# Optimization experiments

Hardware: AMD Instinct MI355X
Metric: run time of the kernel (lower is better)

Reference implementation:

```python
import jax, jax.numpy as jnp
import numpy as np

H = 128  # target_size / hidden_size
D_IN = 2  # input_size - 2 (stard_LSTM slices off last 2 grid coords)
SAMP = 10  # sampling_num (hardcoded stride 10 in forward loop)


def lstm_encode(x, lengths, W_ih, W_hh, b_ih, b_hh):
    # x: [B, T, D_IN]; torch.nn.LSTMCell math, zero initial state
    B, T, _ = x.shape
    xg = jnp.einsum('btd,gd->btg', x, W_ih) + b_ih  # precompute input projections [B,T,4H]

    def step(carry, xt):
        h, c = carry
        g = xt + h @ W_hh.T + b_hh
        i, f, gg, o = jnp.split(g, 4, axis=-1)
        c = jax.nn.sigmoid(f) * c + jax.nn.sigmoid(i) * jnp.tanh(gg)
        h = jax.nn.sigmoid(o) * jnp.tanh(c)
        return (h, c), h

    h0 = jnp.zeros((B, H), x.dtype)
    _, hs = jax.lax.scan(step, (h0, h0), xg.transpose(1, 0, 2))
    outputs = hs.transpose(1, 0, 2)  # [B, T, H]
    emb = outputs[jnp.arange(B), jnp.clip(lengths - 1, 0)]  # last valid step per sequence
    return emb, outputs


def gather_sub(tensor, sub_len):
    # tensor: [B, T, H]; sub_len: [B*SAMP]; row k reads tensor[k//SAMP, sub_len[k]-1]
    rows = jnp.arange(sub_len.shape[0]) // SAMP
    return tensor[rows, jnp.clip(sub_len - 1, 0)]


def exp_neg_dist(a, b):
    return jnp.exp(-jnp.sqrt(jnp.sum((a - b) ** 2, axis=-1)))


def setup_inputs() -> dict:
    key = jax.random.key(0)
    ks = jax.random.split(key, 12)
    B, T, D = 220, 512, 4
    NS = B * SAMP
    rint = lambda k, n: jnp.maximum(jax.random.randint(k, (n,), 0, T), 1).astype(jnp.int64)
    inp = {
        'traj_input': jax.random.normal(ks[0], (B, T, D), jnp.float32),
        'traj_length': rint(ks[1], B),
        'traj_anchor_sub_length': rint(ks[2], NS),
        'traj_farest_sub_length': rint(ks[3], NS),
        'traj_anchor_input': jax.random.normal(ks[4], (B, T, D), jnp.float32),
        'traj_anchor_length': rint(ks[5], B),
        'anchor_sub_length': rint(ks[6], NS),
        'traj_farest_input': jax.random.normal(ks[7], (B, T, D), jnp.float32),
        'traj_farest_length': rint(ks[8], B),
        'farest_sub_length': rint(ks[9], NS),
        'W_ih': jax.random.normal(ks[10], (4 * H, D_IN), jnp.float32) / np.sqrt(H),
        'W_hh': jax.random.normal(ks[11], (4 * H, H), jnp.float32) / np.sqrt(H),
        'b_ih': jnp.zeros((4 * H,), jnp.float32),
        'b_hh': jnp.zeros((4 * H,), jnp.float32),
    }
    return inp


def reference(traj_input, traj_length, traj_anchor_sub_length, traj_farest_sub_length,
              traj_anchor_input, traj_anchor_length, anchor_sub_length,
              traj_farest_input, traj_farest_length, farest_sub_length,
              W_ih, W_hh, b_ih, b_hh):
    # stard_LSTM=True path: cell input drops last 2 coords
    t_emb, t_out = lstm_encode(traj_input[..., :-2], traj_length, W_ih, W_hh, b_ih, b_hh)
    a_emb, a_out = lstm_encode(traj_anchor_input[..., :-2], traj_anchor_length, W_ih, W_hh, b_ih, b_hh)
    f_emb, f_out = lstm_encode(traj_farest_input[..., :-2], traj_farest_length, W_ih, W_hh, b_ih, b_hh)

    ta_sub = gather_sub(t_out, traj_anchor_sub_length)
    tf_sub = gather_sub(t_out, traj_farest_sub_length)
    an_sub = gather_sub(a_out, anchor_sub_length)
    fa_sub = gather_sub(f_out, farest_sub_length)

    anchor_distance = exp_neg_dist(t_emb, a_emb)
    farest_distance = exp_neg_dist(t_emb, f_emb)
    anchor_sub_distance = exp_neg_dist(ta_sub, an_sub)
    farest_sub_distance = exp_neg_dist(tf_sub, fa_sub)
    return (anchor_distance, farest_distance, anchor_sub_distance, farest_sub_distance)
```

## Files before the change

### kernel.cpp

```cpp
#include <hip/hip_runtime.h>

#define H    128
#define T    512
#define DX   4
#define BB   220
#define SAMP 10
#define NS   (BB*SAMP)
#define M    4
#define NBLK 55
#define MAXSLOT 84

typedef _Float16 half8 __attribute__((ext_vector_type(8)));
typedef float    f32x4 __attribute__((ext_vector_type(4)));

#define WS_TEMB 0
#define WS_AEMB (WS_TEMB + BB*H)
#define WS_FEMB (WS_AEMB + BB*H)
#define WS_TA   (WS_FEMB + BB*H)
#define WS_TF   (WS_TA + NS*H)
#define WS_AN   (WS_TF + NS*H)
#define WS_FA   (WS_AN + NS*H)
#define WS_FLAGS (WS_FA + NS*H)

#define LOG2E  1.442695041f
#define LOG2E2 2.885390082f

__device__ static inline float bf2f(unsigned short u) {
  unsigned int i = ((unsigned int)u) << 16;
  return __builtin_bit_cast(float, i);
}
__device__ static inline unsigned short f2bf(float f) {
  unsigned int i = __builtin_bit_cast(unsigned int, f);
  i += 0x7fffu + ((i >> 16) & 1u);
  return (unsigned short)(i >> 16);
}
__device__ static inline float loadF(const void* p, size_t i, int isbf) {
  return isbf ? bf2f(((const unsigned short*)p)[i]) : ((const float*)p)[i];
}
__device__ static inline int loadI(const void* p, int i, int is64) {
  return is64 ? (int)((const unsigned int*)p)[2*(size_t)i] : ((const int*)p)[i];
}
__device__ static inline float frcp(float x) { return __builtin_amdgcn_rcpf(x); }
__device__ static inline float ex2(float x)  { return __builtin_amdgcn_exp2f(x); }
__device__ static inline float sigmY(float y)  { return frcp(1.f + ex2(-y)); }
__device__ static inline float tanhY(float y)  { return 1.f - 2.f*frcp(1.f + ex2(y)); }
__device__ static inline float scrub(float x) { return (x == x) ? x : 0.f; }
__device__ static inline int clampT(int v) { v = v - 1; if (v < 0) v = 0; if (v > T-1) v = T-1; return v; }
__device__ static inline float qsel(f32x4 G, int quad) {
  float g01 = (quad & 1) ? G[1] : G[0];
  float g23 = (quad & 1) ? G[3] : G[2];
  return (quad & 2) ? g23 : g01;
}

__global__ __launch_bounds__(512, 2) void lstm_scan(
    const void* __restrict__ x0_, const void* __restrict__ len0,
    const void* __restrict__ sub_ta, const void* __restrict__ sub_tf,
    const void* __restrict__ x1_, const void* __restrict__ len1,
    const void* __restrict__ sub_an,
    const void* __restrict__ x2_, const void* __restrict__ len2,
    const void* __restrict__ sub_fa,
    const void* __restrict__ Wih, const void* __restrict__ Whh,
    const void* __restrict__ bih, const void* __restrict__ bhh,
    float* __restrict__ ws)
{
  const int e      = blockIdx.y;
  const int s0     = blockIdx.x * M;
  const int tid    = threadIdx.x;
  const int lane   = tid & 63;
  const int w      = tid >> 6;
  const int lo     = lane & 15;
  const int quad   = lane >> 4;

  int fbf, f64;
  {
    const unsigned int* wp = (const unsigned int*)Whh;
    int cnt = 0;
    for (int i = 0; i < 64; ++i) {
      unsigned int lo16 = wp[i] & 0xFFFFu;
      int ex = (int)((lo16 >> 7) & 0xFFu);
      cnt += (ex >= 100 && ex <= 130);
    }
    fbf = (cnt >= 40);
    const unsigned int* l = (const unsigned int*)len0;
    f64 = ((l[1] | l[3] | l[5] | l[7]) == 0u);
    if (blockIdx.x == 0 && blockIdx.y == 0 && tid == 0) {
      int* fo = (int*)(ws + WS_FLAGS); fo[0] = fbf; fo[1] = f64;
    }
  }

  const void* xin  = (e==0) ? x0_ : (e==1 ? x1_ : x2_);
  const void* lenp = (e==0) ? len0 : (e==1 ? len1 : len2);

  __shared__ __align__(16) _Float16 afr[2][4][16][8];
  __shared__ __align__(16) float2 xbf[M][T+2];
  __shared__ __align__(16) _Float16 sbuf[MAXSLOT][H];
  __shared__ int slot_off[MAXSLOT];

  ((unsigned int*)afr)[tid] = 0u;
  for (int i = tid; i < M*T; i += 512) {
    int m = i >> 9, t = i & (T-1);
    size_t base = ((size_t)(s0+m)*T + t) * DX;
    xbf[m][t] = make_float2(loadF(xin, base + 0, fbf), loadF(xin, base + 1, fbf));
  }
  half8 Bf[4][4];
  const int col = w*16 + lo;
  #pragma unroll
  for (int q = 0; q < 4; ++q) {
    const float sc = (q == 2) ? LOG2E2 : LOG2E;
    const int g = q*128 + col;
    #pragma unroll
    for (int kt = 0; kt < 4; ++kt) {
      #pragma unroll
      for (int j = 0; j < 8; ++j) {
        const int k = kt*32 + quad*8 + j;
        Bf[q][kt][j] = (_Float16)(sc * loadF(Whh, (size_t)g*H + k, fbf));
      }
    }
  }
  float wx0[4], wx1[4], bb[4];
  #pragma unroll
  for (int q = 0; q < 4; ++q) {
    const float sc = (q == 2) ? LOG2E2 : LOG2E;
    const int g = q*128 + col;
    wx0[q] = sc * loadF(Wih, (size_t)g*2 + 0, fbf);
    wx1[q] = sc * loadF(Wih, (size_t)g*2 + 1, fbf);
    bb[q]  = sc * (loadF(bih, g, fbf) + loadF(bhh, g, fbf));
  }
  const int nslots = (e == 0) ? M*21 : M*11;
  int myt = -1, mym = 0;
  if (e == 0) {
    if (tid < M*21) {
      int m = tid / 21, j = tid - m*21, sg = s0 + m;
      mym = m;
      int off;
      if (j == 0)       { myt = clampT(loadI(lenp, sg, f64));            off = WS_TEMB + sg*H; }
      else if (j <= 10) { int k = sg*10 + (j-1);  myt = clampT(loadI(sub_ta, k, f64)); off = WS_TA + k*H; }
      else              { int k = sg*10 + (j-11); myt = clampT(loadI(sub_tf, k, f64)); off = WS_TF + k*H; }
      slot_off[tid] = off;
    }
  } else {
    if (tid < M*11) {
      int m = tid / 11, j = tid - m*11, sg = s0 + m;
      mym = m;
      int off;
      if (j == 0) { myt = clampT(loadI(lenp, sg, f64)); off = (e==1 ? WS_AEMB : WS_FEMB) + sg*H; }
      else {
        int k = sg*10 + (j-1);
        if (e == 1) { myt = clampT(loadI(sub_an, k, f64)); off = WS_AN + k*H; }
        else        { myt = clampT(loadI(sub_fa, k, f64)); off = WS_FA + k*H; }
      }
      slot_off[tid] = off;
    }
  }
  __syncthreads();

  float cs = 0.f;
  const int rdchunk = quad*4 + (lo & 3);
  const _Float16* rdb[2] = { &afr[0][0][rdchunk][0], &afr[1][0][rdchunk][0] };
  const int wrkt    = w >> 1;
  const int wrchunk = ((w & 1)*2 + (lo >> 3))*4 + quad;
  const int wrj     = lo & 7;
  _Float16* wrb[2] = { &afr[0][wrkt][wrchunk][wrj], &afr[1][wrkt][wrchunk][wrj] };
  const float2* xrow = &xbf[quad][0];
  const int c0 = 2*lane;
  const int snap_base = (c0 >> 5)*128 + ((c0 >> 3) & 3)*32 + (c0 & 7);

  auto step = [&](int rp, int wp, int t) {
    float2 xv = xrow[t];
    const _Float16* rb = rdb[rp];
    half8 A[4];
    #pragma unroll
    for (int kt = 0; kt < 4; ++kt)
      A[kt] = *(const half8*)(rb + kt*128);

    f32x4 G[4];
    #pragma unroll
    for (int q = 0; q < 4; ++q) G[q] = (f32x4){0.f, 0.f, 0.f, 0.f};
    #pragma unroll
    for (int kt = 0; kt < 4; ++kt)
      #pragma unroll
      for (int q = 0; q < 4; ++q)
        G[q] = __builtin_amdgcn_mfma_f32_16x16x32_f16(A[kt], Bf[q][kt], G[q], 0, 0, 0);

    float R[4];
    #pragma unroll
    for (int q = 0; q < 4; ++q)
      R[q] = qsel(G[q], quad) + bb[q] + wx0[q]*xv.x + wx1[q]*xv.y;

    float sf = sigmY(R[1]);
    float si = sigmY(R[0]);
    float tg = tanhY(R[2]);
    float ig = (si * tg) * LOG2E2;
    cs = sf*cs + ig;
    float tc = tanhY(cs);
    float so = sigmY(R[3]);
    *wrb[wp] = (_Float16)(so * tc);
    __syncthreads();
    unsigned long long mask = __ballot(myt == t);
    if (mask) {
      const _Float16* sb = &afr[wp][0][0][0];
      do {
        int src = __ffsll((unsigned long long)mask) - 1;
        mask &= mask - 1;
        int m    = __shfl(mym, src);
        int slot = w*64 + src;
        unsigned int pk = *(const unsigned int*)(sb + snap_base + m*8);
        *(unsigned int*)&sbuf[slot][c0] = pk;
      } while (mask);
    }
  };

  #pragma unroll 1
  for (int t = 0; t < T; t += 2) {
    step(0, 1, t);
    step(1, 0, t+1);
  }

  __syncthreads();
  for (int i = tid; i < nslots*64; i += 512) {
    int slot = i >> 6, c2 = i & 63;
    unsigned int pk = *(const unsigned int*)&sbuf[slot][2*c2];
    float2 v;
    v.x = (float)__builtin_bit_cast(_Float16, (unsigned short)(pk & 0xFFFFu));
    v.y = (float)__builtin_bit_cast(_Float16, (unsigned short)(pk >> 16));
    *(float2*)(ws + slot_off[slot] + 2*c2) = v;
  }
}

__global__ void dists(const float* __restrict__ ws, void* __restrict__ outv) {
  const int fbf = ((const int*)(ws + WS_FLAGS))[0];
  const int gtid = blockIdx.x*256 + threadIdx.x;
  const int widx = gtid >> 6, lane = gtid & 63;
  const float *pa, *pb;
  if (widx < 220)       { pa = ws + WS_TEMB + (size_t)widx*H;        pb = ws + WS_AEMB + (size_t)widx*H; }
  else if (widx < 440)  { int b = widx-220;  pa = ws + WS_TEMB + (size_t)b*H; pb = ws + WS_FEMB + (size_t)b*H; }
  else if (widx < 2640) { int k = widx-440;  pa = ws + WS_TA + (size_t)k*H;   pb = ws + WS_AN + (size_t)k*H; }
  else                  { int k = widx-2640; pa = ws + WS_TF + (size_t)k*H;   pb = ws + WS_FA + (size_t)k*H; }
  float d0 = pa[lane]    - pb[lane];
  float d1 = pa[lane+64] - pb[lane+64];
  float s  = scrub(d0*d0 + d1*d1);
  #pragma unroll
  for (int off = 32; off > 0; off >>= 1) s += __shfl_down(s, off, 64);
  if (lane == 0) {
    float r = __expf(-sqrtf(s));
    if (fbf) ((unsigned short*)outv)[widx] = f2bf(r);
    else     ((float*)outv)[widx] = r;
  }
}

extern "C" void kernel_launch(void* const* d_in, const int* in_sizes, int n_in,
                              void* d_out, int out_size, void* d_ws, size_t ws_size,
                              hipStream_t stream) {
  float* ws = (float*)d_ws;
  hipLaunchKernelGGL(lstm_scan, dim3(NBLK, 3), dim3(512), 0, stream,
                     d_in[0], d_in[1], d_in[2], d_in[3],
                     d_in[4], d_in[5], d_in[6],
                     d_in[7], d_in[8], d_in[9],
                     d_in[10], d_in[11], d_in[12], d_in[13], ws);
  hipLaunchKernelGGL(dists, dim3(4840*64/256), dim3(256), 0, stream, ws, d_out);
}
```

Measured before the change: 367.6 us.

## Fold input projection into MFMA accumulator and defer snapshots past the barrier

```diff
diff --git a/kernel.cpp b/kernel.cpp
--- a/kernel.cpp
+++ b/kernel.cpp
@@ -46,11 +46,6 @@
 __device__ static inline float tanhY(float y)  { return 1.f - 2.f*frcp(1.f + ex2(y)); }
 __device__ static inline float scrub(float x) { return (x == x) ? x : 0.f; }
 __device__ static inline int clampT(int v) { v = v - 1; if (v < 0) v = 0; if (v > T-1) v = T-1; return v; }
-__device__ static inline float qsel(f32x4 G, int quad) {
-  float g01 = (quad & 1) ? G[1] : G[0];
-  float g23 = (quad & 1) ? G[3] : G[2];
-  return (quad & 2) ? g23 : g01;
-}
 
 __global__ __launch_bounds__(512, 2) void lstm_scan(
     const void* __restrict__ x0_, const void* __restrict__ len0,
@@ -127,7 +122,7 @@
     bb[q]  = sc * (loadF(bih, g, fbf) + loadF(bhh, g, fbf));
   }
   const int nslots = (e == 0) ? M*21 : M*11;
-  int myt = -1, mym = 0;
+  int myt = -2, mym = 0;
   if (e == 0) {
     if (tid < M*21) {
       int m = tid / 21, j = tid - m*21, sg = s0 + m;
@@ -155,8 +150,9 @@
   __syncthreads();
 
   float cs = 0.f;
-  const int rdchunk = quad*4 + (lo & 3);
+  const int rdchunk = quad*4 + (lo >> 2);
   const _Float16* rdb[2] = { &afr[0][0][rdchunk][0], &afr[1][0][rdchunk][0] };
+  const _Float16* sbb[2] = { &afr[0][0][0][0], &afr[1][0][0][0] };
   const int wrkt    = w >> 1;
   const int wrchunk = ((w & 1)*2 + (lo >> 3))*4 + quad;
   const int wrj     = lo & 7;
@@ -165,40 +161,10 @@
   const int c0 = 2*lane;
   const int snap_base = (c0 >> 5)*128 + ((c0 >> 3) & 3)*32 + (c0 & 7);
 
-  auto step = [&](int rp, int wp, int t) {
-    float2 xv = xrow[t];
-    const _Float16* rb = rdb[rp];
-    half8 A[4];
-    #pragma unroll
-    for (int kt = 0; kt < 4; ++kt)
-      A[kt] = *(const half8*)(rb + kt*128);
-
-    f32x4 G[4];
-    #pragma unroll
-    for (int q = 0; q < 4; ++q) G[q] = (f32x4){0.f, 0.f, 0.f, 0.f};
-    #pragma unroll
-    for (int kt = 0; kt < 4; ++kt)
-      #pragma unroll
-      for (int q = 0; q < 4; ++q)
-        G[q] = __builtin_amdgcn_mfma_f32_16x16x32_f16(A[kt], Bf[q][kt], G[q], 0, 0, 0);
-
-    float R[4];
-    #pragma unroll
-    for (int q = 0; q < 4; ++q)
-      R[q] = qsel(G[q], quad) + bb[q] + wx0[q]*xv.x + wx1[q]*xv.y;
-
-    float sf = sigmY(R[1]);
-    float si = sigmY(R[0]);
-    float tg = tanhY(R[2]);
-    float ig = (si * tg) * LOG2E2;
-    cs = sf*cs + ig;
-    float tc = tanhY(cs);
-    float so = sigmY(R[3]);
-    *wrb[wp] = (_Float16)(so * tc);
-    __syncthreads();
-    unsigned long long mask = __ballot(myt == t);
+  auto snap = [&](int tq, int rp) {
+    unsigned long long mask = __ballot(myt == tq);
     if (mask) {
-      const _Float16* sb = &afr[wp][0][0][0];
+      const _Float16* sb = sbb[rp];
       do {
         int src = __ffsll((unsigned long long)mask) - 1;
         mask &= mask - 1;
@@ -210,11 +176,51 @@
     }
   };
 
+  auto step = [&](int rp, int wp, int t) {
+    float2 xv = xrow[t];
+    const _Float16* rb = rdb[rp];
+    half8 A[4];
+    #pragma unroll
+    for (int kt = 0; kt < 4; ++kt)
+      A[kt] = *(const half8*)(rb + kt*128);
+
+    float pre[4];
+    #pragma unroll
+    for (int q = 0; q < 4; ++q)
+      pre[q] = bb[q] + wx0[q]*xv.x + wx1[q]*xv.y;
+    f32x4 G[4];
+    #pragma unroll
+    for (int q = 0; q < 4; ++q)
+      G[q] = (f32x4){pre[q], pre[q], pre[q], pre[q]};
+
+    __builtin_amdgcn_s_setprio(1);
+    #pragma unroll
+    for (int kt = 0; kt < 4; ++kt)
+      #pragma unroll
+      for (int q = 0; q < 4; ++q)
+        G[q] = __builtin_amdgcn_mfma_f32_16x16x32_f16(A[kt], Bf[q][kt], G[q], 0, 0, 0);
+    __builtin_amdgcn_s_setprio(0);
+
+    snap(t-1, rp);
+
+    float sf = sigmY(G[1][0]);
+    float si = sigmY(G[0][0]);
+    float tg = tanhY(G[2][0]);
+    float ig = (si * tg) * LOG2E2;
+    cs = sf*cs + ig;
+    float tc = tanhY(cs);
+    float so = sigmY(G[3][0]);
+    *wrb[wp] = (_Float16)(so * tc);
+    __syncthreads();
+  };
+
   #pragma unroll 1
   for (int t = 0; t < T; t += 2) {
     step(0, 1, t);
     step(1, 0, t+1);
   }
+
+  snap(T-1, 0);
 
   __syncthreads();
   for (int i = tid; i < nslots*64; i += 512) {
```

Result: slower. 399.2 us (+8.6%).
